# Performance work log

Hardware: AMD Instinct MI355X
Metric: run time of the kernel (lower is better)

## Reference

```python
import jax, jax.numpy as jnp
import numpy as np
from jax.scipy.special import erf, erfinv

N_OBS = 8192   # number of observations
N_LOC = 2048   # number of spatial locations (q)


def setup_inputs() -> dict:
    key = jax.random.key(0)
    k1, k2, k3, k4 = jax.random.split(key, 4)
    # random 2-D coordinates -> symmetric pairwise squared-distance matrix (zero diag)
    coords = jax.random.uniform(k1, (N_LOC, 2), dtype=jnp.float32) * 10.0
    dist_matrix = jnp.sum((coords[:, None, :] - coords[None, :, :]) ** 2, axis=-1)  # [q,q]
    Z_idx = jax.random.randint(k2, (N_OBS,), 0, N_LOC)                              # location id per obs
    y_true = jax.random.normal(k3, (N_OBS, 1), dtype=jnp.float32)
    y_pred = jax.random.normal(k4, (N_OBS, 1), dtype=jnp.float32) * 0.5
    return {
        "y_true": y_true,
        "y_pred": y_pred,
        "Z_idx": Z_idx,
        "dist_matrix": dist_matrix,
        "sig2e": jnp.array([1.0], dtype=jnp.float32),
        "sig2bs": jnp.array([0.5], dtype=jnp.float32),
        "lengthscale": jnp.array([2.0], dtype=jnp.float32),
    }


def _inverse_gaussian_cdf(u):
    # tf.math.erfinv(2*clip(u,1e-5,1-1e-5)-1) * sqrt(2)
    return erfinv(2.0 * jnp.clip(u, 1e-5, 1.0 - 1e-5) - 1.0) * jnp.sqrt(2.0)


def reference(y_true, y_pred, Z_idx, dist_matrix, sig2e, sig2bs, lengthscale):
    N = y_true.shape[0]
    q = dist_matrix.shape[0]
    dt = y_true.dtype
    # getD: exponential distance kernel over locations  D = sig2b * exp(-M / (2*ell))
    D = sig2bs[0] * jnp.exp(-dist_matrix / (2.0 * lengthscale[0]))          # [q,q]
    # getZ: dense one-hot design matrix (sparse.to_dense of SparseTensor of ones)
    Z = jax.nn.one_hot(Z_idx, q, dtype=dt)                                   # [N,q]
    # V_batch: V = Z D Z' + sig2e * I
    V = Z @ (D @ Z.T) + sig2e[0] * jnp.eye(N, dtype=dt)                      # [N,N]
    sd = jnp.sqrt(jnp.diagonal(V))                                           # sd_sqrt_V
    R = V / (sd[:, None] * sd[None, :])                                      # correlation matrix
    # Gaussian marginal: sig2 = sig2e + sig2b (diag of V)
    sig2 = sig2e[0] + sig2bs[0]
    resid = y_true - y_pred                                                  # [N,1]
    # distribution.cdf_batch: standard normal CDF of resid / sqrt(sig2)
    u = 0.5 * (erf(resid / jnp.sqrt(2.0 * sig2)) + 1.0)
    m = _inverse_gaussian_cdf(u)                                             # [N,1]
    # distribution.sum_log_pdf_batch: sum of Gaussian log-pdf
    sum_log_pdf = jnp.sum(-0.5 * jnp.log(2.0 * jnp.pi * sig2) - resid ** 2 / (2.0 * sig2))
    # solve + logdet via a single Cholesky of the correlation matrix
    L = jnp.linalg.cholesky(R)
    V_inv_m = jax.scipy.linalg.cho_solve((L, True), m)                       # R^{-1} m
    logdet = 2.0 * jnp.sum(jnp.log(jnp.diagonal(L)))                         # logdet(V) - 2*sum(log sd)
    mV_invm = m.T @ V_inv_m                                                  # [1,1]
    mtm = m.T @ m                                                            # [1,1]
    total_loss = 0.5 * logdet + 0.5 * mV_invm - 0.5 * mtm + 0.5 * sum_log_pdf
    return total_loss  # [1,1]
```

## Files before the change

kernel.cpp:

```cpp
#include <hip/hip_runtime.h>
#include <math.h>

#define Q 2048
#define NOBS 8192

__device__ __forceinline__ float rl(float v, int l) {
  return __int_as_float(__builtin_amdgcn_readlane(__float_as_int(v), l));
}

__device__ __forceinline__ float block_sum256(float v, volatile float* red) {
  int tid = threadIdx.x;
#pragma unroll
  for (int o = 32; o > 0; o >>= 1) v += __shfl_down(v, o);
  __syncthreads();
  if ((tid & 63) == 0) red[tid >> 6] = v;
  __syncthreads();
  return red[0] + red[1] + red[2] + red[3];
}

__device__ __forceinline__ float chol64_reg(float rr[64], int lane) {
  float dv = 1.0f;
#pragma unroll
  for (int j = 0; j < 64; ++j) {
    float vjj = rl(rr[j], j);
    float invd = rsqrtf(vjj);
    float lij = rr[j] * invd;
    rr[j] = lij;
    if (lane == j) dv = lij;
#pragma unroll
    for (int k = j + 1; k < 64; ++k) rr[k] -= lij * rl(lij, k);
  }
  return dv;
}

__device__ __forceinline__ void panel_solve(float* sh, const float* LT,
                                            const float* invDs, int lane) {
  float rr2[64];
#pragma unroll
  for (int k = 0; k < 64; ++k) rr2[k] = sh[k * 68 + lane];
  __builtin_amdgcn_s_setprio(1);
#pragma unroll
  for (int p = 0; p < 64; ++p) {
    float xp = rr2[p] * invDs[p];
    rr2[p] = xp;
#pragma unroll
    for (int k4 = 0; k4 < 16; ++k4) {
      if (k4 * 4 + 3 > p) {
        float4 l4 = *(const float4*)&LT[p * 64 + k4 * 4];
        rr2[k4 * 4 + 0] -= xp * l4.x;
        rr2[k4 * 4 + 1] -= xp * l4.y;
        rr2[k4 * 4 + 2] -= xp * l4.z;
        rr2[k4 * 4 + 3] -= xp * l4.w;
      }
    }
  }
  __builtin_amdgcn_s_setprio(0);
#pragma unroll
  for (int k = 0; k < 64; ++k) sh[k * 68 + lane] = rr2[k];
}

__device__ __forceinline__ void zsolve(const float* LT, const float* invDs,
                                       const float* zin, float* z1s, int lane) {
  float rr3[64];
#pragma unroll
  for (int p = 0; p < 64; ++p) rr3[p] = LT[p * 64 + lane];
  float a = zin[lane];
  float myinv = invDs[lane];
#pragma unroll
  for (int p = 0; p < 64; ++p) {
    float xp = rl(a, p) * rl(myinv, p);
    if (lane > p) a -= xp * rr3[p];
  }
  z1s[lane] = a * myinv;
}

__global__ __launch_bounds__(256) void obs_kernel(
    const float* __restrict__ yt, const float* __restrict__ yp,
    const int* __restrict__ zidx, const float* __restrict__ s2e_p,
    const float* __restrict__ s2b_p, float* __restrict__ t,
    int* __restrict__ cnt, float* __restrict__ scal) {
  __shared__ float red[4];
  int i = blockIdx.x * 256 + threadIdx.x;
  float s2e = s2e_p[0], s2b = s2b_p[0];
  float sig2 = s2e + s2b;
  float r = yt[i] - yp[i];
  float e = erff(r * rsqrtf(2.0f * sig2));
  float u = 0.5f * (e + 1.0f);
  u = fminf(fmaxf(u, 1e-5f), 1.0f - 1e-5f);
  float m = erfinvf(2.0f * u - 1.0f) * 1.4142135623730951f;
  float slp = -0.5f * logf(2.0f * 3.14159265358979f * sig2) - r * r / (2.0f * sig2);
  int z = zidx[i];
  atomicAdd(&t[z], m);
  atomicAdd(&cnt[z], 1);
  float s1 = block_sum256(slp, red);
  float s2 = block_sum256(m * m, red);
  if (threadIdx.x == 0) {
    atomicAdd(&scal[0], s1);
    atomicAdd(&scal[1], s2);
  }
}

__global__ __launch_bounds__(256) void build_mv(
    const float* __restrict__ dist, const float* __restrict__ s2e_p,
    const float* __restrict__ s2b_p, const float* __restrict__ ell_p,
    const int* __restrict__ cnt, const float* __restrict__ t,
    float* __restrict__ G, float* __restrict__ z, float* __restrict__ scal) {
  __shared__ float red[4];
  int j = blockIdx.x;
  float s2e = s2e_p[0], s2b = s2b_p[0], ell = ell_p[0];
  float sig2 = s2e + s2b;
  float ratio = s2b / sig2;
  float diag = s2e / sig2;
  float inv2ell = 1.0f / (2.0f * ell);
  float cj = (float)cnt[j];
  const float* drow = dist + (size_t)j * Q;
  float* grow = G + (size_t)j * Q;
  float s = 0.0f;
  for (int k = threadIdx.x; k < Q; k += 256) {
    float e = expf(-drow[k] * inv2ell);
    s += e * t[k];
    float g = sqrtf(cj * (float)cnt[k]) * (ratio * e);
    if (j == k) g += diag;
    grow[k] = g;
  }
  float tot = block_sum256(s, red);
  if (threadIdx.x == 0) {
    float wj = ratio * tot;
    z[j] = sqrtf(cj) * wj;
    atomicAdd(&scal[2], t[j] * wj);
  }
}

__global__ __launch_bounds__(64, 1) void potrf_first(
    const float* __restrict__ G, float* __restrict__ dsA,
    float* __restrict__ scal) {
  int lane = threadIdx.x;
  float rr[64];
  const float* row = G + (size_t)lane * Q;
#pragma unroll
  for (int k4 = 0; k4 < 16; ++k4) {
    float4 v = *(const float4*)(row + k4 * 4);
    rr[k4 * 4 + 0] = v.x; rr[k4 * 4 + 1] = v.y;
    rr[k4 * 4 + 2] = v.z; rr[k4 * 4 + 3] = v.w;
  }
  float dv = chol64_reg(rr, lane);
#pragma unroll
  for (int k4 = 0; k4 < 16; ++k4) {
    float4 st;
    st.x = rr[k4 * 4 + 0]; st.y = rr[k4 * 4 + 1];
    st.z = rr[k4 * 4 + 2]; st.w = rr[k4 * 4 + 3];
    *(float4*)(dsA + lane * 64 + k4 * 4) = st;
  }
  float lg = logf(dv);
#pragma unroll
  for (int o = 32; o > 0; o >>= 1) lg += __shfl_down(lg, o);
  if (lane == 0) atomicAdd(&scal[3], lg);
}

__global__ __launch_bounds__(256, 1) void estep(
    float* __restrict__ G, float* __restrict__ z, float* __restrict__ z1,
    float* __restrict__ scal, const float* __restrict__ dsR,
    float* __restrict__ dsW, int j0) {
  __shared__ __align__(16) float shA[64 * 68];
  __shared__ __align__(16) float shB[64 * 68];
  __shared__ __align__(16) float LT[64 * 64];
  __shared__ float invDs[64];
  __shared__ float z1s[64];
  int tid = threadIdx.x, bx = blockIdx.x;
  int lane = tid & 63, wv = tid >> 6;
  int tx = tid & 15, ty = tid >> 4;
  int j1 = j0 + 64;

  bool isjob0 = (bx == 0);
  int tjob = bx - 1;
  if (!isjob0 && tjob == 0) return;

  int R0, C0;
  bool sym;
  if (isjob0) {
    R0 = j1; C0 = j1; sym = true;
  } else {
    int bi = (int)((sqrtf(8.0f * (float)tjob + 1.0f) - 1.0f) * 0.5f);
    while ((bi + 1) * (bi + 2) / 2 <= tjob) ++bi;
    while (bi * (bi + 1) / 2 > tjob) --bi;
    int bk = tjob - bi * (bi + 1) / 2;
    R0 = j1 + bi * 64; C0 = j1 + bk * 64; sym = (bi == bk);
  }

#pragma unroll
  for (int it = 0; it < 4; ++it) {
    int idx = it * 256 + tid;
    int r = idx >> 4, c4 = (idx & 15) * 4;
    float4 v = *(const float4*)(dsR + r * 64 + c4);
    LT[(c4 + 0) * 64 + r] = (c4 + 0 < r) ? v.x : 0.0f;
    LT[(c4 + 1) * 64 + r] = (c4 + 1 < r) ? v.y : 0.0f;
    LT[(c4 + 2) * 64 + r] = (c4 + 2 < r) ? v.z : 0.0f;
    LT[(c4 + 3) * 64 + r] = (c4 + 3 < r) ? v.w : 0.0f;
    if (r >= c4 && r < c4 + 4) {
      float d = (r == c4) ? v.x : (r == c4 + 1) ? v.y : (r == c4 + 2) ? v.z : v.w;
      invDs[r] = 1.0f / d;
    }
  }
#pragma unroll
  for (int it = 0; it < 4; ++it) {
    int idx = it * 256 + tid;
    int r = idx >> 4, c4 = (idx & 15) * 4;
    float4 v = *(const float4*)(G + (size_t)(R0 + r) * Q + j0 + c4);
    shA[(c4 + 0) * 68 + r] = v.x; shA[(c4 + 1) * 68 + r] = v.y;
    shA[(c4 + 2) * 68 + r] = v.z; shA[(c4 + 3) * 68 + r] = v.w;
    if (!sym) {
      float4 u = *(const float4*)(G + (size_t)(C0 + r) * Q + j0 + c4);
      shB[(c4 + 0) * 68 + r] = u.x; shB[(c4 + 1) * 68 + r] = u.y;
      shB[(c4 + 2) * 68 + r] = u.z; shB[(c4 + 3) * 68 + r] = u.w;
    }
  }
  __syncthreads();

  if (wv == 0) {
    panel_solve(shA, LT, invDs, lane);
  } else if (wv == 1) {
    if (!sym) panel_solve(shB, LT, invDs, lane);
    else      zsolve(LT, invDs, z + j0, z1s, lane);
  }
  __syncthreads();

  if (isjob0 && wv == 1) z1[j0 + lane] = z1s[lane];

  const float* sB = sym ? shA : shB;
  float acc[4][4] = {{0.f}};
#pragma unroll 8
  for (int p = 0; p < 64; ++p) {
    float4 a4 = *(const float4*)&shA[p * 68 + ty * 4];
    float4 b4 = *(const float4*)&sB[p * 68 + tx * 4];
    float av[4] = {a4.x, a4.y, a4.z, a4.w};
    float bv[4] = {b4.x, b4.y, b4.z, b4.w};
#pragma unroll
    for (int i = 0; i < 4; ++i)
#pragma unroll
      for (int jj = 0; jj < 4; ++jj) acc[i][jj] += av[i] * bv[jj];
  }

  if (isjob0) {
#pragma unroll
    for (int i = 0; i < 4; ++i) {
      const float* gp = G + (size_t)(j1 + ty * 4 + i) * Q + j1 + tx * 4;
      float4 g = *(const float4*)gp;
      shB[(ty * 4 + i) * 68 + tx * 4 + 0] = g.x - acc[i][0];
      shB[(ty * 4 + i) * 68 + tx * 4 + 1] = g.y - acc[i][1];
      shB[(ty * 4 + i) * 68 + tx * 4 + 2] = g.z - acc[i][2];
      shB[(ty * 4 + i) * 68 + tx * 4 + 3] = g.w - acc[i][3];
    }
    __syncthreads();
    if (wv == 0) {
      float rr[64];
#pragma unroll
      for (int k4 = 0; k4 < 16; ++k4) {
        float4 v = *(const float4*)&shB[lane * 68 + k4 * 4];
        rr[k4 * 4 + 0] = v.x; rr[k4 * 4 + 1] = v.y;
        rr[k4 * 4 + 2] = v.z; rr[k4 * 4 + 3] = v.w;
      }
      __builtin_amdgcn_s_setprio(1);
      float dv = chol64_reg(rr, lane);
      __builtin_amdgcn_s_setprio(0);
#pragma unroll
      for (int k4 = 0; k4 < 16; ++k4) {
        float4 st;
        st.x = rr[k4 * 4 + 0]; st.y = rr[k4 * 4 + 1];
        st.z = rr[k4 * 4 + 2]; st.w = rr[k4 * 4 + 3];
        *(float4*)(dsW + lane * 64 + k4 * 4) = st;
      }
      float lg = logf(dv);
#pragma unroll
      for (int o = 32; o > 0; o >>= 1) lg += __shfl_down(lg, o);
      if (lane == 0) atomicAdd(&scal[3], lg);
    } else if (wv == 1) {
      float zs = 0.f;
#pragma unroll 8
      for (int p = 0; p < 64; ++p) zs += shA[p * 68 + lane] * z1s[p];
      z[j1 + lane] -= zs;
    }
    return;
  }

  if (sym && wv == 0) {
    float zs = 0.f;
#pragma unroll 8
    for (int p = 0; p < 64; ++p) zs += shA[p * 68 + lane] * z1s[p];
    z[R0 + lane] -= zs;
  }
#pragma unroll
  for (int i = 0; i < 4; ++i) {
    float* gp = G + (size_t)(R0 + ty * 4 + i) * Q + C0 + tx * 4;
    float4 g = *(const float4*)gp;
    g.x -= acc[i][0]; g.y -= acc[i][1];
    g.z -= acc[i][2]; g.w -= acc[i][3];
    *(float4*)gp = g;
  }
}

__global__ __launch_bounds__(256) void final_assemble(
    const float* __restrict__ z, const float* __restrict__ z1,
    const float* __restrict__ ds31, const float* __restrict__ scal,
    const float* __restrict__ s2e_p, const float* __restrict__ s2b_p,
    float* __restrict__ out) {
  __shared__ float red[4];
  __shared__ float z1last[64];
  int tid = threadIdx.x;
  if (tid < 64) {
    int lane = tid;
    float rr3[64];
#pragma unroll
    for (int k4 = 0; k4 < 16; ++k4) {
      float4 v = *(const float4*)(ds31 + lane * 64 + k4 * 4);
      rr3[k4 * 4 + 0] = v.x; rr3[k4 * 4 + 1] = v.y;
      rr3[k4 * 4 + 2] = v.z; rr3[k4 * 4 + 3] = v.w;
    }
    float myinv = 1.0f / rr3[lane];
    float a = z[Q - 64 + lane];
#pragma unroll
    for (int p = 0; p < 64; ++p) {
      float xp = rl(a, p) * rl(myinv, p);
      if (lane > p) a -= xp * rr3[p];
    }
    z1last[lane] = a * myinv;
  }
  __syncthreads();
  float bv = 0.f;
  for (int i = tid; i < Q; i += 256) {
    float zi = (i < Q - 64) ? z1[i] : z1last[i - (Q - 64)];
    bv += zi * zi;
  }
  float bvs = block_sum256(bv, red);
  if (tid == 0) {
    float s2e = s2e_p[0], s2b = s2b_p[0];
    float sig2 = s2e + s2b;
    float c = s2e / sig2;
    float slp = scal[0], mtm = scal[1];
    float tw = scal[2], sl = scal[3];
    float tty = (tw - bvs) / c;
    float mrm = (mtm - tty) / c;
    float logdetR = (float)(NOBS - Q) * logf(c) + 2.0f * sl;
    out[0] = 0.5f * logdetR + 0.5f * mrm - 0.5f * mtm + 0.5f * slp;
  }
}

extern "C" void kernel_launch(void* const* d_in, const int* in_sizes, int n_in,
                              void* d_out, int out_size, void* d_ws, size_t ws_size,
                              hipStream_t stream) {
  const float* yt   = (const float*)d_in[0];
  const float* yp   = (const float*)d_in[1];
  const int*   zidx = (const int*)d_in[2];
  const float* dist = (const float*)d_in[3];
  const float* s2e  = (const float*)d_in[4];
  const float* s2b  = (const float*)d_in[5];
  const float* ell  = (const float*)d_in[6];

  float* ws   = (float*)d_ws;
  float* G    = ws;
  float* z    = ws + (size_t)Q * Q;
  float* t    = z + Q;
  int*   cntv = (int*)(t + Q);
  float* scal = t + 2 * Q;
  float* z1   = scal + 8;
  float* dsA  = z1 + Q;
  float* dsB  = dsA + 4096;

  hipMemsetAsync(t, 0, (2 * Q + 8) * sizeof(float), stream);

  obs_kernel<<<NOBS / 256, 256, 0, stream>>>(yt, yp, zidx, s2e, s2b, t, cntv, scal);
  build_mv<<<Q, 256, 0, stream>>>(dist, s2e, s2b, ell, cntv, t, G, z, scal);

  potrf_first<<<1, 64, 0, stream>>>(G, dsA, scal);

  for (int s = 0; s <= 30; ++s) {
    int m = 31 - s;
    int ntile = m * (m + 1) / 2;
    const float* dsR = (s & 1) ? dsB : dsA;
    float* dsW = (s & 1) ? dsA : dsB;
    estep<<<1 + ntile, 256, 0, stream>>>(G, z, z1, scal, dsR, dsW, s * 64);
  }

  final_assemble<<<1, 256, 0, stream>>>(z, z1, dsB, scal, s2e, s2b,
                                        (float*)d_out);
}
```

Baseline: 973.6 us.

## Replace per-panel triangular solves with explicit inverse of diagonal Cholesky block

The diagonal 64x64 Cholesky factor is now inverted explicitly (inv64_reg) once per step and stored in place of the factor. Trailing panel updates and the z forward solve then become dense GEMM/GEMV products with the inverse rather than serial triangular solves on one or two waves, which spreads the work across all 256 threads. The cost is a serial inversion on the critical-path diagonal block, an extra shared-memory transpose pass, and slightly different numerical stability.

```diff
diff --git a/kernel.cpp b/kernel.cpp
--- a/kernel.cpp
+++ b/kernel.cpp
@@ -33,45 +33,16 @@
   return dv;
 }
 
-__device__ __forceinline__ void panel_solve(float* sh, const float* LT,
-                                            const float* invDs, int lane) {
-  float rr2[64];
-#pragma unroll
-  for (int k = 0; k < 64; ++k) rr2[k] = sh[k * 68 + lane];
-  __builtin_amdgcn_s_setprio(1);
-#pragma unroll
-  for (int p = 0; p < 64; ++p) {
-    float xp = rr2[p] * invDs[p];
-    rr2[p] = xp;
-#pragma unroll
-    for (int k4 = 0; k4 < 16; ++k4) {
-      if (k4 * 4 + 3 > p) {
-        float4 l4 = *(const float4*)&LT[p * 64 + k4 * 4];
-        rr2[k4 * 4 + 0] -= xp * l4.x;
-        rr2[k4 * 4 + 1] -= xp * l4.y;
-        rr2[k4 * 4 + 2] -= xp * l4.z;
-        rr2[k4 * 4 + 3] -= xp * l4.w;
-      }
-    }
-  }
-  __builtin_amdgcn_s_setprio(0);
-#pragma unroll
-  for (int k = 0; k < 64; ++k) sh[k * 68 + lane] = rr2[k];
-}
-
-__device__ __forceinline__ void zsolve(const float* LT, const float* invDs,
-                                       const float* zin, float* z1s, int lane) {
-  float rr3[64];
-#pragma unroll
-  for (int p = 0; p < 64; ++p) rr3[p] = LT[p * 64 + lane];
-  float a = zin[lane];
-  float myinv = invDs[lane];
-#pragma unroll
-  for (int p = 0; p < 64; ++p) {
-    float xp = rl(a, p) * rl(myinv, p);
-    if (lane > p) a -= xp * rr3[p];
-  }
-  z1s[lane] = a * myinv;
+__device__ __forceinline__ void inv64_reg(const float rr[64], float myinv,
+                                          float wcol[64], int lane) {
+#pragma unroll
+  for (int r = 0; r < 64; ++r) {
+    float s = (lane == r) ? 1.0f : 0.0f;
+#pragma unroll
+    for (int p = 0; p < 64; ++p)
+      if (p < r) s -= rl(rr[p], r) * wcol[p];
+    wcol[r] = s * rl(myinv, r);
+  }
 }
 
 __global__ __launch_bounds__(256) void obs_kernel(
@@ -144,17 +115,19 @@
     rr[k4 * 4 + 2] = v.z; rr[k4 * 4 + 3] = v.w;
   }
   float dv = chol64_reg(rr, lane);
+  float lg = logf(dv);
+#pragma unroll
+  for (int o = 32; o > 0; o >>= 1) lg += __shfl_down(lg, o);
+  if (lane == 0) atomicAdd(&scal[3], lg);
+  float wcol[64];
+  inv64_reg(rr, 1.0f / dv, wcol, lane);
 #pragma unroll
   for (int k4 = 0; k4 < 16; ++k4) {
     float4 st;
-    st.x = rr[k4 * 4 + 0]; st.y = rr[k4 * 4 + 1];
-    st.z = rr[k4 * 4 + 2]; st.w = rr[k4 * 4 + 3];
+    st.x = wcol[k4 * 4 + 0]; st.y = wcol[k4 * 4 + 1];
+    st.z = wcol[k4 * 4 + 2]; st.w = wcol[k4 * 4 + 3];
     *(float4*)(dsA + lane * 64 + k4 * 4) = st;
   }
-  float lg = logf(dv);
-#pragma unroll
-  for (int o = 32; o > 0; o >>= 1) lg += __shfl_down(lg, o);
-  if (lane == 0) atomicAdd(&scal[3], lg);
 }
 
 __global__ __launch_bounds__(256, 1) void estep(
@@ -163,9 +136,9 @@
     float* __restrict__ dsW, int j0) {
   __shared__ __align__(16) float shA[64 * 68];
   __shared__ __align__(16) float shB[64 * 68];
-  __shared__ __align__(16) float LT[64 * 64];
-  __shared__ float invDs[64];
+  __shared__ __align__(16) float shW[64 * 68];
   __shared__ float z1s[64];
+  __shared__ float z2s[64];
   int tid = threadIdx.x, bx = blockIdx.x;
   int lane = tid & 63, wv = tid >> 6;
   int tx = tid & 15, ty = tid >> 4;
@@ -190,16 +163,9 @@
 #pragma unroll
   for (int it = 0; it < 4; ++it) {
     int idx = it * 256 + tid;
-    int r = idx >> 4, c4 = (idx & 15) * 4;
-    float4 v = *(const float4*)(dsR + r * 64 + c4);
-    LT[(c4 + 0) * 64 + r] = (c4 + 0 < r) ? v.x : 0.0f;
-    LT[(c4 + 1) * 64 + r] = (c4 + 1 < r) ? v.y : 0.0f;
-    LT[(c4 + 2) * 64 + r] = (c4 + 2 < r) ? v.z : 0.0f;
-    LT[(c4 + 3) * 64 + r] = (c4 + 3 < r) ? v.w : 0.0f;
-    if (r >= c4 && r < c4 + 4) {
-      float d = (r == c4) ? v.x : (r == c4 + 1) ? v.y : (r == c4 + 2) ? v.z : v.w;
-      invDs[r] = 1.0f / d;
-    }
+    int c = idx >> 4, r4 = (idx & 15) * 4;
+    float4 w = *(const float4*)(dsR + c * 64 + r4);
+    *(float4*)&shW[c * 68 + r4] = w;
   }
 #pragma unroll
   for (int it = 0; it < 4; ++it) {
@@ -214,24 +180,60 @@
       shB[(c4 + 2) * 68 + r] = u.z; shB[(c4 + 3) * 68 + r] = u.w;
     }
   }
-  __syncthreads();
-
-  if (wv == 0) {
-    panel_solve(shA, LT, invDs, lane);
-  } else if (wv == 1) {
-    if (!sym) panel_solve(shB, LT, invDs, lane);
-    else      zsolve(LT, invDs, z + j0, z1s, lane);
-  }
-  __syncthreads();
-
-  if (isjob0 && wv == 1) z1[j0 + lane] = z1s[lane];
-
-  const float* sB = sym ? shA : shB;
+  if (sym && tid < 64) z2s[tid] = z[j0 + tid];
+  __syncthreads();
+
+  if (sym && wv == 1) {
+    float a = 0.f;
+#pragma unroll
+    for (int c = 0; c < 64; ++c) a += shW[c * 68 + lane] * z2s[c];
+    z1s[lane] = a;
+  }
+
+  float acc1[4][4] = {{0.f}};
+  float acc2[4][4] = {{0.f}};
+#pragma unroll 8
+  for (int c = 0; c < 64; ++c) {
+    float4 a4 = *(const float4*)&shA[c * 68 + ty * 4];
+    float4 w4 = *(const float4*)&shW[c * 68 + tx * 4];
+    float av[4] = {a4.x, a4.y, a4.z, a4.w};
+    float wv4[4] = {w4.x, w4.y, w4.z, w4.w};
+#pragma unroll
+    for (int i = 0; i < 4; ++i)
+#pragma unroll
+      for (int jj = 0; jj < 4; ++jj) acc1[i][jj] += av[i] * wv4[jj];
+    if (!sym) {
+      float4 b4 = *(const float4*)&shB[c * 68 + ty * 4];
+      float bv[4] = {b4.x, b4.y, b4.z, b4.w};
+#pragma unroll
+      for (int i = 0; i < 4; ++i)
+#pragma unroll
+        for (int jj = 0; jj < 4; ++jj) acc2[i][jj] += bv[i] * wv4[jj];
+    }
+  }
+  __syncthreads();
+
+#pragma unroll
+  for (int jj = 0; jj < 4; ++jj) {
+    float4 s1;
+    s1.x = acc1[0][jj]; s1.y = acc1[1][jj];
+    s1.z = acc1[2][jj]; s1.w = acc1[3][jj];
+    *(float4*)&shA[(tx * 4 + jj) * 68 + ty * 4] = s1;
+    if (!sym) {
+      float4 s2;
+      s2.x = acc2[0][jj]; s2.y = acc2[1][jj];
+      s2.z = acc2[2][jj]; s2.w = acc2[3][jj];
+      *(float4*)&shB[(tx * 4 + jj) * 68 + ty * 4] = s2;
+    }
+  }
+  __syncthreads();
+
+  const float* sB2 = sym ? shA : shB;
   float acc[4][4] = {{0.f}};
 #pragma unroll 8
-  for (int p = 0; p < 64; ++p) {
-    float4 a4 = *(const float4*)&shA[p * 68 + ty * 4];
-    float4 b4 = *(const float4*)&sB[p * 68 + tx * 4];
+  for (int j = 0; j < 64; ++j) {
+    float4 a4 = *(const float4*)&shA[j * 68 + ty * 4];
+    float4 b4 = *(const float4*)&sB2[j * 68 + tx * 4];
     float av[4] = {a4.x, a4.y, a4.z, a4.w};
     float bv[4] = {b4.x, b4.y, b4.z, b4.w};
 #pragma unroll
@@ -245,47 +247,51 @@
     for (int i = 0; i < 4; ++i) {
       const float* gp = G + (size_t)(j1 + ty * 4 + i) * Q + j1 + tx * 4;
       float4 g = *(const float4*)gp;
-      shB[(ty * 4 + i) * 68 + tx * 4 + 0] = g.x - acc[i][0];
-      shB[(ty * 4 + i) * 68 + tx * 4 + 1] = g.y - acc[i][1];
-      shB[(ty * 4 + i) * 68 + tx * 4 + 2] = g.z - acc[i][2];
-      shB[(ty * 4 + i) * 68 + tx * 4 + 3] = g.w - acc[i][3];
+      shW[(ty * 4 + i) * 68 + tx * 4 + 0] = g.x - acc[i][0];
+      shW[(ty * 4 + i) * 68 + tx * 4 + 1] = g.y - acc[i][1];
+      shW[(ty * 4 + i) * 68 + tx * 4 + 2] = g.z - acc[i][2];
+      shW[(ty * 4 + i) * 68 + tx * 4 + 3] = g.w - acc[i][3];
     }
     __syncthreads();
+    if (wv == 1) {
+      float zs = 0.f;
+#pragma unroll 8
+      for (int j = 0; j < 64; ++j) zs += shA[j * 68 + lane] * z1s[j];
+      z[j1 + lane] -= zs;
+      z1[j0 + lane] = z1s[lane];
+    }
     if (wv == 0) {
       float rr[64];
 #pragma unroll
       for (int k4 = 0; k4 < 16; ++k4) {
-        float4 v = *(const float4*)&shB[lane * 68 + k4 * 4];
+        float4 v = *(const float4*)&shW[lane * 68 + k4 * 4];
         rr[k4 * 4 + 0] = v.x; rr[k4 * 4 + 1] = v.y;
         rr[k4 * 4 + 2] = v.z; rr[k4 * 4 + 3] = v.w;
       }
       __builtin_amdgcn_s_setprio(1);
       float dv = chol64_reg(rr, lane);
+      float lg = logf(dv);
+#pragma unroll
+      for (int o = 32; o > 0; o >>= 1) lg += __shfl_down(lg, o);
+      if (lane == 0) atomicAdd(&scal[3], lg);
+      float wcol[64];
+      inv64_reg(rr, 1.0f / dv, wcol, lane);
       __builtin_amdgcn_s_setprio(0);
 #pragma unroll
       for (int k4 = 0; k4 < 16; ++k4) {
         float4 st;
-        st.x = rr[k4 * 4 + 0]; st.y = rr[k4 * 4 + 1];
-        st.z = rr[k4 * 4 + 2]; st.w = rr[k4 * 4 + 3];
+        st.x = wcol[k4 * 4 + 0]; st.y = wcol[k4 * 4 + 1];
+        st.z = wcol[k4 * 4 + 2]; st.w = wcol[k4 * 4 + 3];
         *(float4*)(dsW + lane * 64 + k4 * 4) = st;
       }
-      float lg = logf(dv);
-#pragma unroll
-      for (int o = 32; o > 0; o >>= 1) lg += __shfl_down(lg, o);
-      if (lane == 0) atomicAdd(&scal[3], lg);
-    } else if (wv == 1) {
-      float zs = 0.f;
-#pragma unroll 8
-      for (int p = 0; p < 64; ++p) zs += shA[p * 68 + lane] * z1s[p];
-      z[j1 + lane] -= zs;
     }
     return;
   }
 
-  if (sym && wv == 0) {
+  if (sym && wv == 1) {
     float zs = 0.f;
 #pragma unroll 8
-    for (int p = 0; p < 64; ++p) zs += shA[p * 68 + lane] * z1s[p];
+    for (int j = 0; j < 64; ++j) zs += shA[j * 68 + lane] * z1s[j];
     z[R0 + lane] -= zs;
   }
 #pragma unroll
@@ -305,24 +311,16 @@
     float* __restrict__ out) {
   __shared__ float red[4];
   __shared__ float z1last[64];
+  __shared__ float z2l[64];
   int tid = threadIdx.x;
+  if (tid < 64) z2l[tid] = z[Q - 64 + tid];
+  __syncthreads();
   if (tid < 64) {
     int lane = tid;
-    float rr3[64];
-#pragma unroll
-    for (int k4 = 0; k4 < 16; ++k4) {
-      float4 v = *(const float4*)(ds31 + lane * 64 + k4 * 4);
-      rr3[k4 * 4 + 0] = v.x; rr3[k4 * 4 + 1] = v.y;
-      rr3[k4 * 4 + 2] = v.z; rr3[k4 * 4 + 3] = v.w;
-    }
-    float myinv = 1.0f / rr3[lane];
-    float a = z[Q - 64 + lane];
-#pragma unroll
-    for (int p = 0; p < 64; ++p) {
-      float xp = rl(a, p) * rl(myinv, p);
-      if (lane > p) a -= xp * rr3[p];
-    }
-    z1last[lane] = a * myinv;
+    float a = 0.f;
+#pragma unroll
+    for (int c = 0; c < 64; ++c) a += ds31[c * 64 + lane] * z2l[c];
+    z1last[lane] = a;
   }
   __syncthreads();
   float bv = 0.f;
```

Result: slower. 3.304 ms (+239.3%).
